# Performance work log

Hardware: AMD Instinct MI355X
Metric: run time of the kernel (lower is better)

## Reference

```python
import jax, jax.numpy as jnp
import numpy as np

CHANNELS = 8
IN_CHANNELS = 8
MASK_OUT_STRIDE = 4
WEIGHT_NUMS = [(IN_CHANNELS + 2) * CHANNELS, CHANNELS * CHANNELS, CHANNELS * 1]
BIAS_NUMS = [CHANNELS, CHANNELS, 1]
SOI = jnp.array([8.0, 16.0, 32.0, 64.0, 128.0], dtype=jnp.float32)
EPS = 1e-5


def compute_locations(h, w, stride):
    # (x, y) center of each stride-sized cell, row-major (y outer, x inner)
    sx = jnp.arange(w, dtype=jnp.float32) * stride + stride // 2
    sy = jnp.arange(h, dtype=jnp.float32) * stride + stride // 2
    yy, xx = jnp.meshgrid(sy, sx, indexing='ij')
    return jnp.stack([xx.reshape(-1), yy.reshape(-1)], axis=-1)  # [H*W, 2]


def aligned_bilinear(t, factor):
    # Matches AdelaiDet aligned_bilinear: replicate-pad right/bottom, bilinear
    # upsample align_corners=True to (f*h+1, f*w+1), replicate-pad top/left by
    # f//2, crop to (f*h, f*w).
    if factor == 1:
        return t
    n, c, h, w = t.shape
    t = jnp.pad(t, ((0, 0), (0, 0), (0, 1), (0, 1)), mode='edge')  # [n,c,h+1,w+1]
    oh, ow = factor * h + 1, factor * w + 1
    ys = jnp.arange(oh, dtype=jnp.float32) / factor  # align_corners mapping
    xs = jnp.arange(ow, dtype=jnp.float32) / factor
    y0 = jnp.floor(ys).astype(jnp.int32)
    x0 = jnp.floor(xs).astype(jnp.int32)
    y1 = jnp.minimum(y0 + 1, h)
    x1 = jnp.minimum(x0 + 1, w)
    wy = (ys - y0.astype(jnp.float32)).astype(t.dtype)
    wx = (xs - x0.astype(jnp.float32)).astype(t.dtype)
    ty = t[:, :, y0, :] * (1.0 - wy)[None, None, :, None] + t[:, :, y1, :] * wy[None, None, :, None]
    out = ty[:, :, :, x0] * (1.0 - wx) + ty[:, :, :, x1] * wx
    p = factor // 2
    out = jnp.pad(out, ((0, 0), (0, 0), (p, 0), (p, 0)), mode='edge')
    return out[:, :, :oh - 1, :ow - 1]


def parse_dynamic_params(params):
    n = params.shape[0]
    splits = jnp.split(params, np.cumsum(WEIGHT_NUMS + BIAS_NUMS)[:-1], axis=1)
    w0 = splits[0].reshape(n, CHANNELS, IN_CHANNELS + 2)
    w1 = splits[1].reshape(n, CHANNELS, CHANNELS)
    w2 = splits[2].reshape(n, 1, CHANNELS)
    b0 = splits[3].reshape(n, CHANNELS)
    b1 = splits[4].reshape(n, CHANNELS)
    b2 = splits[5].reshape(n, 1)
    return (w0, w1, w2), (b0, b1, b2)


def setup_inputs() -> dict:
    key = jax.random.key(0)
    ks = jax.random.split(key, 6)
    N, H, W = 2, 100, 136
    n_inst = 500
    return {
        'mask_feats': jax.random.normal(ks[0], (N, IN_CHANNELS, H, W), dtype=jnp.float32),
        'mask_head_params': jax.random.normal(ks[1], (n_inst, 169), dtype=jnp.float32),
        'locations_inst': jax.random.uniform(ks[2], (n_inst, 2), dtype=jnp.float32),
        'gt_bitmasks': jax.random.uniform(ks[3], (n_inst, 1, 2 * H, 2 * W), dtype=jnp.float32),
        'im_inds': jax.random.randint(ks[4], (n_inst,), 0, N, dtype=jnp.int64 if jax.config.jax_enable_x64 else jnp.int32),
        'fpn_levels': jax.random.randint(ks[5], (n_inst,), 0, 5, dtype=jnp.int64 if jax.config.jax_enable_x64 else jnp.int32),
        'mask_feat_stride': 8,
    }


def reference(mask_feats, mask_head_params, locations_inst, gt_bitmasks, im_inds, fpn_levels, mask_feat_stride):
    N, Cin, H, W = mask_feats.shape
    n = mask_head_params.shape[0]
    # relative coordinates, normalized by per-instance size-of-interest
    locs = compute_locations(H, W, mask_feat_stride)                 # [HW, 2]
    rel = locations_inst[:, None, :] - locs[None, :, :]              # [n, HW, 2]
    rel = jnp.transpose(rel, (0, 2, 1))                              # [n, 2, HW]
    soi = SOI[fpn_levels]                                            # [n]
    rel = (rel / soi[:, None, None]).astype(mask_feats.dtype)
    feats = mask_feats[im_inds].reshape(n, Cin, H * W)               # gather per instance
    x = jnp.concatenate([rel, feats], axis=1)                        # [n, Cin+2, HW]
    # per-instance 1x1 conv stack == batched small GEMMs
    (w0, w1, w2), (b0, b1, b2) = parse_dynamic_params(mask_head_params)
    x = jax.nn.relu(jnp.einsum('nci,nip->ncp', w0, x) + b0[:, :, None])
    x = jax.nn.relu(jnp.einsum('nci,nip->ncp', w1, x) + b1[:, :, None])
    x = jnp.einsum('nci,nip->ncp', w2, x) + b2[:, :, None]           # [n, 1, HW]
    logits = x.reshape(n, 1, H, W)
    logits = aligned_bilinear(logits, mask_feat_stride // MASK_OUT_STRIDE)
    scores = jax.nn.sigmoid(logits)                                  # [n, 1, 2H, 2W]
    # dice loss
    xs = scores.reshape(n, -1)
    t = gt_bitmasks.reshape(n, -1)
    inter = jnp.sum(xs * t, axis=1)
    union = jnp.sum(xs * xs, axis=1) + jnp.sum(t * t, axis=1) + EPS
    loss = 1.0 - 2.0 * inter / union
    return jnp.mean(loss)
```

## Files before the change

kernel.cpp:

```cpp
#include <hip/hip_runtime.h>
#include <math.h>

#define CIN      8
#define H_IN     100
#define W_IN     136
#define NPIX     (H_IN * W_IN)
#define OH       (2 * H_IN)
#define OW       (2 * W_IN)
#define ONPIX    (OH * OW)
#define NPARAMS  169
#define EPSV     1e-5f
#define NSLICE   4
#define KG4      34
#define KGROUPS  34
#define TASKS_B  (25 * KGROUPS)


__device__ __forceinline__ float sigmoidf_fast(float x) {
    float e = __expf(-x);
    return __builtin_amdgcn_rcpf(1.f + e);
}

__global__ __launch_bounds__(256, 5)
void mask_head_fused(const float* __restrict__ mask_feats,
                     const float* __restrict__ params,
                     const float* __restrict__ locs,
                     const float* __restrict__ gt,
                     const int*   __restrict__ im_inds,
                     const int*   __restrict__ fpn_levels,
                     float*       __restrict__ partials)
{
    const int inst  = blockIdx.x >> 2;
    const int slice = blockIdx.x & 3;
    const int tid   = threadIdx.x;

    const int r_start = (slice == 0) ? 0 : 25 * slice - 1;
    const int nrows   = (slice == 0) ? 25 : 26;
    const int ntask   = nrows * KG4;

    __shared__ float s_logit[26 * W_IN];
    __shared__ float s_red[12];

    const float* __restrict__ wp = params + (size_t)inst * NPARAMS;

    const int   im  = im_inds[inst];
    const int   lvl = fpn_levels[inst];
    const float inv_soi = exp2f(-(float)(3 + lvl));
    const float lx = locs[inst * 2 + 0];
    const float ly = locs[inst * 2 + 1];
    const float dx8 = 8.f * inv_soi;

    const float* feat = mask_feats + (size_t)im * (CIN * NPIX);
    const int goff = r_start * W_IN;

    #pragma unroll 1
    for (int it = 0; it < 4; ++it) {
        const int t = it * 256 + tid;
        if (t < ntask) {
            const int r  = t / KG4;
            const int k  = t - r * KG4;
            const int lpx = r * W_IN + 4 * k;
            const float* fb = feat + (goff + lpx);

            float4 f[8];
            #pragma unroll
            for (int c = 0; c < CIN; ++c)
                f[c] = *(const float4*)(fb + c * NPIX);

            float in0[4];
            in0[0] = (lx - (float)(32 * k + 4)) * inv_soi;
            in0[1] = in0[0] - dx8;
            in0[2] = in0[1] - dx8;
            in0[3] = in0[2] - dx8;
            const float in1 = (ly - (float)((r_start + r) * 8 + 4)) * inv_soi;

            float o4[4];

#define DO_PX(J, COMP)                                                        \
            {                                                                 \
                float aj[8];                                                  \
                _Pragma("unroll")                                             \
                for (int o = 0; o < 8; ++o)                                   \
                    aj[o] = fmaf(wp[o * 10], in0[J],                          \
                                 fmaf(wp[o * 10 + 1], in1, wp[152 + o]));     \
                _Pragma("unroll")                                             \
                for (int c = 0; c < 8; ++c) {                                 \
                    _Pragma("unroll")                                         \
                    for (int o = 0; o < 8; ++o)                               \
                        aj[o] = fmaf(wp[o * 10 + 2 + c], f[c].COMP, aj[o]);   \
                }                                                             \
                _Pragma("unroll")                                             \
                for (int o = 0; o < 8; ++o)                                   \
                    aj[o] = fmaxf(aj[o], 0.f);                                \
                float acc = wp[168];                                          \
                _Pragma("unroll")                                             \
                for (int o = 0; o < 8; ++o) {                                 \
                    float tt = wp[160 + o];                                   \
                    _Pragma("unroll")                                         \
                    for (int i = 0; i < 8; ++i)                               \
                        tt = fmaf(wp[80 + o * 8 + i], aj[i], tt);             \
                    acc = fmaf(wp[144 + o], fmaxf(tt, 0.f), acc);             \
                }                                                             \
                o4[J] = acc;                                                  \
            }

            DO_PX(0, x)
            DO_PX(1, y)
            DO_PX(2, z)
            DO_PX(3, w)
#undef DO_PX

            float4 ov = {o4[0], o4[1], o4[2], o4[3]};
            *(float4*)(s_logit + lpx) = ov;
        }
    }

    __syncthreads();

    float inter = 0.f, ssum = 0.f, tsum = 0.f;
    const float* gtp = gt + (size_t)inst * ONPIX;
    const int pair_base = 25 * slice;

    #pragma unroll 1
    for (int base = 0; base < TASKS_B; base += 256) {
        const int task = base + tid;
        if (task < TASKS_B) {
            const int pl = task / KGROUPS;
            const int k  = task - pl * KGROUPS;
            const int pg = pair_base + pl;
            const int er = pg - r_start;
            const int pr = (pg > 0 ? pg - 1 : 0) - r_start;
            const float* E = s_logit + er * W_IN;
            const float* P = s_logit + pr * W_IN;
            const int c0  = 4 * k;
            const int cm1 = (k > 0) ? c0 - 1 : 0;

            const float* g0 = gtp + (size_t)(2 * pg) * OW + 8 * k;
            const float4 ga = *(const float4*)(g0);
            const float4 gb = *(const float4*)(g0 + 4);
            const float4 gc = *(const float4*)(g0 + OW);
            const float4 gd = *(const float4*)(g0 + OW + 4);
            const float4 e4 = *(const float4*)(E + c0);
            const float  em = E[cm1];
            const float4 p4 = *(const float4*)(P + c0);
            const float  pm = P[cm1];

            const float ecur[4] = {e4.x, e4.y, e4.z, e4.w};
            const float pcur[4] = {p4.x, p4.y, p4.z, p4.w};
            const float gav[8] = {ga.x, ga.y, ga.z, ga.w, gb.x, gb.y, gb.z, gb.w};
            const float gex[8] = {gc.x, gc.y, gc.z, gc.w, gd.x, gd.y, gd.z, gd.w};

            float Se_prev = em;
            float Sa_prev = 0.5f * (em + pm);
            #pragma unroll
            for (int j = 0; j < 4; ++j) {
                const float Se = ecur[j];
                const float Sa = 0.5f * (ecur[j] + pcur[j]);
                {
                    float s = sigmoidf_fast(0.5f * (Sa_prev + Sa));
                    float t2 = gav[2 * j];
                    inter = fmaf(s, t2, inter); ssum = fmaf(s, s, ssum); tsum = fmaf(t2, t2, tsum);
                    s = sigmoidf_fast(Sa);
                    t2 = gav[2 * j + 1];
                    inter = fmaf(s, t2, inter); ssum = fmaf(s, s, ssum); tsum = fmaf(t2, t2, tsum);
                }
                {
                    float s = sigmoidf_fast(0.5f * (Se_prev + Se));
                    float t2 = gex[2 * j];
                    inter = fmaf(s, t2, inter); ssum = fmaf(s, s, ssum); tsum = fmaf(t2, t2, tsum);
                    s = sigmoidf_fast(Se);
                    t2 = gex[2 * j + 1];
                    inter = fmaf(s, t2, inter); ssum = fmaf(s, s, ssum); tsum = fmaf(t2, t2, tsum);
                }
                Se_prev = Se;
                Sa_prev = Sa;
            }
        }
    }

    #pragma unroll
    for (int off = 32; off > 0; off >>= 1) {
        inter += __shfl_down(inter, off, 64);
        ssum  += __shfl_down(ssum,  off, 64);
        tsum  += __shfl_down(tsum,  off, 64);
    }
    const int wid = tid >> 6;
    if ((tid & 63) == 0) {
        s_red[wid * 3 + 0] = inter;
        s_red[wid * 3 + 1] = ssum;
        s_red[wid * 3 + 2] = tsum;
    }
    __syncthreads();
    if (tid == 0) {
        float I = 0.f, S = 0.f, T = 0.f;
        #pragma unroll
        for (int w = 0; w < 4; ++w) {
            I += s_red[w * 3 + 0];
            S += s_red[w * 3 + 1];
            T += s_red[w * 3 + 2];
        }
        partials[blockIdx.x * 3 + 0] = I;
        partials[blockIdx.x * 3 + 1] = S;
        partials[blockIdx.x * 3 + 2] = T;
    }
}

__global__ __launch_bounds__(512)
void loss_mean_kernel(const float* __restrict__ partials, float* __restrict__ out, int n)
{
    __shared__ float s_red[8];
    float v = 0.f;
    for (int i = threadIdx.x; i < n; i += 512) {
        float I = 0.f, S = 0.f, T = 0.f;
        #pragma unroll
        for (int s = 0; s < NSLICE; ++s) {
            const float* p = partials + (size_t)(i * NSLICE + s) * 3;
            I += p[0];
            S += p[1];
            T += p[2];
        }
        v += 1.f - 2.f * I / (S + T + EPSV);
    }
    #pragma unroll
    for (int off = 32; off > 0; off >>= 1) v += __shfl_down(v, off, 64);
    const int wid = threadIdx.x >> 6;
    if ((threadIdx.x & 63) == 0) s_red[wid] = v;
    __syncthreads();
    if (threadIdx.x == 0) {
        float s = 0.f;
        #pragma unroll
        for (int w = 0; w < 8; ++w) s += s_red[w];
        out[0] = s / (float)n;
    }
}

extern "C" void kernel_launch(void* const* d_in, const int* in_sizes, int n_in,
                              void* d_out, int out_size, void* d_ws, size_t ws_size,
                              hipStream_t stream)
{
    const float* mask_feats = (const float*)d_in[0];
    const float* params     = (const float*)d_in[1];
    const float* locs       = (const float*)d_in[2];
    const float* gt         = (const float*)d_in[3];
    const int*   im_inds    = (const int*)d_in[4];
    const int*   fpn_levels = (const int*)d_in[5];

    const int n = in_sizes[4];
    float* partials = (float*)d_ws;

    mask_head_fused<<<n * NSLICE, 256, 0, stream>>>(mask_feats, params, locs, gt,
                                                    im_inds, fpn_levels, partials);
    loss_mean_kernel<<<1, 512, 0, stream>>>(partials, (float*)d_out, n);
}
```

Measured before the change: 182.2 us.

## Split fused mask head into separate logits and dice kernels via global buffer

Replaces the single fused kernel, which kept per-slice logits in shared memory and recomputed one halo row per slice, with two kernels. The first writes the logits for all instances to a workspace buffer in global memory. The second reads them back for bilinear upsampling and the dice reduction. This removes the halo recomputation and the shared-memory footprint, but adds a global write and read of the logits plus an extra kernel launch.

```diff
diff --git a/kernel.cpp b/kernel.cpp
--- a/kernel.cpp
+++ b/kernel.cpp
@@ -12,6 +12,7 @@
 #define EPSV     1e-5f
 #define NSLICE   4
 #define KG4      34
+#define TASKS_A  (25 * KG4)
 #define KGROUPS  34
 #define TASKS_B  (25 * KGROUPS)
 
@@ -21,25 +22,19 @@
     return __builtin_amdgcn_rcpf(1.f + e);
 }
 
-__global__ __launch_bounds__(256, 5)
-void mask_head_fused(const float* __restrict__ mask_feats,
-                     const float* __restrict__ params,
-                     const float* __restrict__ locs,
-                     const float* __restrict__ gt,
-                     const int*   __restrict__ im_inds,
-                     const int*   __restrict__ fpn_levels,
-                     float*       __restrict__ partials)
+
+__global__ __launch_bounds__(256, 4)
+void logits_kernel(const float* __restrict__ mask_feats,
+                   const float* __restrict__ params,
+                   const float* __restrict__ locs,
+                   const int*   __restrict__ im_inds,
+                   const int*   __restrict__ fpn_levels,
+                   float*       __restrict__ logits)
 {
     const int inst  = blockIdx.x >> 2;
     const int slice = blockIdx.x & 3;
     const int tid   = threadIdx.x;
-
-    const int r_start = (slice == 0) ? 0 : 25 * slice - 1;
-    const int nrows   = (slice == 0) ? 25 : 26;
-    const int ntask   = nrows * KG4;
-
-    __shared__ float s_logit[26 * W_IN];
-    __shared__ float s_red[12];
+    const int r_start = 25 * slice;
 
     const float* __restrict__ wp = params + (size_t)inst * NPARAMS;
 
@@ -52,11 +47,12 @@
 
     const float* feat = mask_feats + (size_t)im * (CIN * NPIX);
     const int goff = r_start * W_IN;
+    float* lg = logits + (size_t)inst * NPIX + goff;
 
     #pragma unroll 1
     for (int it = 0; it < 4; ++it) {
         const int t = it * 256 + tid;
-        if (t < ntask) {
+        if (t < TASKS_A) {
             const int r  = t / KG4;
             const int k  = t - r * KG4;
             const int lpx = r * W_IN + 4 * k;
@@ -111,15 +107,27 @@
 #undef DO_PX
 
             float4 ov = {o4[0], o4[1], o4[2], o4[3]};
-            *(float4*)(s_logit + lpx) = ov;
-        }
-    }
-
-    __syncthreads();
+            *(float4*)(lg + lpx) = ov;
+        }
+    }
+}
+
+__global__ __launch_bounds__(256, 5)
+void dice_kernel(const float* __restrict__ logits,
+                 const float* __restrict__ gt,
+                 float*       __restrict__ partials)
+{
+    const int inst = blockIdx.x >> 2;
+    const int q    = blockIdx.x & 3;
+    const int tid  = threadIdx.x;
+    const int pair_base = 25 * q;
+
+    __shared__ float s_red[12];
+
+    const float* lgp = logits + (size_t)inst * NPIX;
+    const float* gtp = gt + (size_t)inst * ONPIX;
 
     float inter = 0.f, ssum = 0.f, tsum = 0.f;
-    const float* gtp = gt + (size_t)inst * ONPIX;
-    const int pair_base = 25 * slice;
 
     #pragma unroll 1
     for (int base = 0; base < TASKS_B; base += 256) {
@@ -128,10 +136,8 @@
             const int pl = task / KGROUPS;
             const int k  = task - pl * KGROUPS;
             const int pg = pair_base + pl;
-            const int er = pg - r_start;
-            const int pr = (pg > 0 ? pg - 1 : 0) - r_start;
-            const float* E = s_logit + er * W_IN;
-            const float* P = s_logit + pr * W_IN;
+            const float* E = lgp + (size_t)pg * W_IN;
+            const float* P = lgp + (size_t)(pg > 0 ? pg - 1 : 0) * W_IN;
             const int c0  = 4 * k;
             const int cm1 = (k > 0) ? c0 - 1 : 0;
 
@@ -246,9 +252,12 @@
     const int*   fpn_levels = (const int*)d_in[5];
 
     const int n = in_sizes[4];
+
     float* partials = (float*)d_ws;
-
-    mask_head_fused<<<n * NSLICE, 256, 0, stream>>>(mask_feats, params, locs, gt,
-                                                    im_inds, fpn_levels, partials);
+    float* logits   = (float*)((char*)d_ws + (32 << 10));
+
+    logits_kernel<<<n * NSLICE, 256, 0, stream>>>(mask_feats, params, locs,
+                                                  im_inds, fpn_levels, logits);
+    dice_kernel<<<n * NSLICE, 256, 0, stream>>>(logits, gt, partials);
     loss_mean_kernel<<<1, 512, 0, stream>>>(partials, (float*)d_out, n);
 }
```

Result: slower. 212.3 us (+16.6%).
